# Optimization experiments

Measured on AMD Instinct MI355X. Metric: run time of the kernel, lower is better.

## Reference

```python
import jax, jax.numpy as jnp
import numpy as np

BETA = 0.04
EPS_LOW = 0.2
EPS_HIGH = 0.2
TEMPERATURE = 1.0


def setup_inputs() -> dict:
    key = jax.random.key(0)
    ks = jax.random.split(key, 8)
    B, S, H, V = 4, 1024, 2048, 32000
    return {
        "_input": jax.random.normal(ks[0], (B, S, H), dtype=jnp.float32),
        "lin_weight": jax.random.normal(ks[1], (V, H), dtype=jnp.float32) * 0.02,
        "bias": jax.random.normal(ks[2], (V,), dtype=jnp.float32) * 0.02,
        "selected_token_ids": jax.random.randint(ks[3], (B, S), 0, V),
        "attention_mask": jnp.ones((B, S), dtype=jnp.float32),
        "advantages": jax.random.normal(ks[4], (B,), dtype=jnp.float32),
        "ref_per_token_logps": -jnp.abs(jax.random.normal(ks[5], (B, S), dtype=jnp.float32)),
        "old_per_token_logps": -jnp.abs(jax.random.normal(ks[6], (B, S), dtype=jnp.float32)),
    }


def reference(_input, lin_weight, bias, selected_token_ids, attention_mask,
              advantages, ref_per_token_logps, old_per_token_logps):
    B, S, H = _input.shape
    # fused linear projection to vocab logits: [B,S,V]
    logits = (jnp.einsum("bsh,vh->bsv", _input, lin_weight) + bias) / TEMPERATURE
    log_probs = jax.nn.log_softmax(logits, axis=-1)
    per_token_logps = jnp.take_along_axis(
        log_probs, selected_token_ids[..., None], axis=-1)[..., 0]  # [B,S]

    log_ratio = per_token_logps - old_per_token_logps
    seq_len = jnp.clip(attention_mask.sum(-1), 1.0, None)
    seq_level_log_weight = jax.lax.stop_gradient(
        (log_ratio * attention_mask).sum(-1) / seq_len)[:, None]  # [B,1]

    log_importance_weights = (per_token_logps -
                              jax.lax.stop_gradient(per_token_logps) +
                              seq_level_log_weight)
    coef_1 = jnp.exp(log_importance_weights)
    coef_2 = jnp.clip(coef_1, 1.0 - EPS_LOW, 1.0 + EPS_HIGH)
    adv = advantages[:, None]
    per_token_loss = -jnp.minimum(coef_1 * adv, coef_2 * adv)

    # k3 KL penalty (beta != 0, use_ref_model=True)
    d = ref_per_token_logps - per_token_logps
    kl_div = jnp.exp(d) - d - 1.0
    per_token_loss = per_token_loss + BETA * kl_div

    # loss_type == 'grpo'
    loss = ((per_token_loss * attention_mask).sum(-1) / seq_len).sum() / B
    return loss
```

## Files before the change

kernel.cpp:

```cpp
#include <hip/hip_runtime.h>
#include <hip/hip_bf16.h>

#define BETA_C 0.04f
#define EPS_LOW_C 0.2f
#define EPS_HIGH_C 0.2f

static constexpr int B_ = 4, S_ = 1024, H_ = 2048, V_ = 32000;
static constexpr int M_ = B_ * S_;
static constexpr int BM = 256, BN = 256, BK = 64;
static constexpr int NRB = M_ / BM;
static constexpr int NCB = V_ / BN;
static constexpr int NT  = H_ / BK;

typedef __attribute__((ext_vector_type(8))) short short8;
typedef __attribute__((ext_vector_type(4))) float f32x4;

__device__ __forceinline__ unsigned short f2bf(float f) {
    unsigned u = __builtin_bit_cast(unsigned, f);
    unsigned r = 0x7FFFu + ((u >> 16) & 1u);
    return (unsigned short)((u + r) >> 16);
}

__device__ __forceinline__ void gload_lds16(const unsigned short* g, unsigned short* l) {
    __builtin_amdgcn_global_load_lds(
        (const __attribute__((address_space(1))) unsigned int*)g,
        (__attribute__((address_space(3))) unsigned int*)l, 16, 0, 0);
}

__global__ void cvt_kernel(const float* __restrict__ in, unsigned short* __restrict__ out, int n4) {
    int i = blockIdx.x * blockDim.x + threadIdx.x;
    int stride = gridDim.x * blockDim.x;
    for (; i < n4; i += stride) {
        float4 v = reinterpret_cast<const float4*>(in)[i];
        ushort4 o;
        o.x = f2bf(v.x); o.y = f2bf(v.y); o.z = f2bf(v.z); o.w = f2bf(v.w);
        reinterpret_cast<ushort4*>(out)[i] = o;
    }
}

__global__ __launch_bounds__(512, 2) void gemm_lse_kernel(
    const unsigned short* __restrict__ A,
    const unsigned short* __restrict__ W,
    const float* __restrict__ bias,
    const int* __restrict__ sel,
    float* __restrict__ partials,
    float* __restrict__ sel_logit)
{
    __shared__ __attribute__((aligned(128))) char lds[163840];

    const int bid = blockIdx.x;
    const int swz = (bid & 7) * (NRB * NCB / 8) + (bid >> 3);
    const int brow = swz % NRB;
    const int bcol = swz / NRB;
    const int tid  = threadIdx.x;
    const int lane = tid & 63;
    const int wv   = tid >> 6;
    const int wm   = wv >> 2;
    const int wn   = wv & 3;
    const int l15  = lane & 15, lg = lane >> 4;

    int aBase[2], bBase[2];
    #pragma unroll
    for (int ks = 0; ks < 2; ++ks) {
        const int sw = ((ks * 4 + lg) ^ (l15 & 7)) << 4;
        aBase[ks] = (wm * 128 + l15) * 128 + sw;
        bBase[ks] = (wn * 64 + l15) * 128 + sw;
    }
    int sByte[2][2];
    #pragma unroll
    for (int i = 0; i < 2; ++i)
        #pragma unroll
        for (int h = 0; h < 2; ++h) {
            int c = i * 512 + tid;
            int r = (c >> 3) + h * 128;
            int gg = (c & 7) ^ (r & 7);
            sByte[i][h] = (r * H_ + gg * 8) * 2;
        }

    const unsigned short* Ab = A + (long)brow * BM * H_;
    const unsigned short* Wb = W + (long)bcol * BN * H_;

    f32x4 acc[8][4] = {};
    short8 af0[2][2], af1[2][2], af2[2][2], af3[2][2], bfr[4][2];

#define STG(gb, bufoff, h, kt) \
    { _Pragma("unroll") \
      for (int i_ = 0; i_ < 2; ++i_) \
          gload_lds16((const unsigned short*)((const char*)(gb) + sByte[i_][h] + (kt) * 2), \
                      (unsigned short*)(lds + (bufoff) + (h) * 16384 + (i_ * 512 + tid) * 16)); }

#define RDA(abuf, q, dst) \
    { _Pragma("unroll") \
      for (int mi_ = 0; mi_ < 2; ++mi_) \
      _Pragma("unroll") \
      for (int ks_ = 0; ks_ < 2; ++ks_) \
          dst[mi_][ks_] = *(const short8*)(lds + (abuf) + ((q) * 2 + mi_) * 2048 + aBase[ks_]); }

#define RDB(bbuf) \
    { _Pragma("unroll") \
      for (int n_ = 0; n_ < 4; ++n_) \
      _Pragma("unroll") \
      for (int ks_ = 0; ks_ < 2; ++ks_) \
          bfr[n_][ks_] = *(const short8*)(lds + (bbuf) + n_ * 2048 + bBase[ks_]); }

#define MM(q, afr) \
    __builtin_amdgcn_s_setprio(1); \
    _Pragma("unroll") \
    for (int ks_ = 0; ks_ < 2; ++ks_) \
    _Pragma("unroll") \
    for (int mi_ = 0; mi_ < 2; ++mi_) \
    _Pragma("unroll") \
    for (int n_ = 0; n_ < 4; ++n_) \
        acc[(q) * 2 + mi_][n_] = __builtin_amdgcn_mfma_f32_16x16x32_bf16( \
            afr[mi_][ks_], bfr[n_][ks_], acc[(q) * 2 + mi_][n_], 0, 0, 0); \
    __builtin_amdgcn_s_setprio(0);

#define LGKM(n) asm volatile("s_waitcnt lgkmcnt(" #n ")" ::: "memory"); \
    __builtin_amdgcn_sched_barrier(0);
#define VMC(n)  asm volatile("s_waitcnt vmcnt(" #n ")" ::: "memory");
#define BAR     { __builtin_amdgcn_s_barrier(); __builtin_amdgcn_sched_barrier(0); }
#define SCB     __builtin_amdgcn_sched_barrier(0);

    STG(Ab, 0, 0, 0)       STG(Ab, 0, 1, 0)
    STG(Wb, 65536, 0, 0)   STG(Wb, 65536, 1, 0)
    STG(Wb, 98304, 0, 64)  STG(Wb, 98304, 1, 64)
    VMC(4)
    BAR

    #pragma unroll
    for (int t = 0; t < NT; ++t) {
        const int aR = (t & 1) * 32768;
        const int aW = ((t + 1) & 1) * 32768;
        const int bR = 65536 + (t % 3) * 32768;
        const int bW = 65536 + ((t + 2) % 3) * 32768;
        const int ktA = ((t + 1) * BK) & (H_ - 1);
        const int ktB = ((t + 2) * BK) & (H_ - 1);

        RDB(bR) RDA(aR, 0, af0)
        SCB
        RDA(aR, 1, af1)
        SCB
        STG(Ab, aW, 0, ktA) STG(Ab, aW, 1, ktA)
        STG(Wb, bW, 0, ktB) STG(Wb, bW, 1, ktB)
        LGKM(4)
        MM(0, af0)
        RDA(aR, 2, af2)
        SCB
        LGKM(4)
        MM(1, af1)
        RDA(aR, 3, af3)
        SCB
        LGKM(4)
        MM(2, af2)
        LGKM(0)
        MM(3, af3)
        VMC(4)
        BAR
    }

    VMC(0)
    __syncthreads();

    float* sums = (float*)lds;
    const int colb = bcol * BN + wn * 64 + l15;
    float bv[4];
    #pragma unroll
    for (int n = 0; n < 4; ++n) bv[n] = bias[colb + n * 16];

    #pragma unroll
    for (int m = 0; m < 8; ++m) {
        #pragma unroll
        for (int j = 0; j < 4; ++j) {
            const long grow = (long)brow * BM + wm * 128 + m * 16 + lg * 4 + j;
            const int stok = sel[grow];
            float s = 0.f;
            #pragma unroll
            for (int n = 0; n < 4; ++n) {
                float logit = acc[m][n][j] + bv[n];
                s += __expf(logit);
                if (stok == colb + n * 16) sel_logit[grow] = logit;
            }
            s += __shfl_xor(s, 1); s += __shfl_xor(s, 2);
            s += __shfl_xor(s, 4); s += __shfl_xor(s, 8);
            if (l15 == 0) sums[(wm * 128 + m * 16 + lg * 4 + j) * 4 + wn] = s;
        }
    }
    __syncthreads();
    if (tid < BM) {
        float tot = sums[tid * 4 + 0] + sums[tid * 4 + 1] + sums[tid * 4 + 2] + sums[tid * 4 + 3];
        partials[((long)brow * BM + tid) * NCB + bcol] = tot;
    }
#undef STG
#undef RDA
#undef RDB
#undef MM
#undef LGKM
#undef VMC
#undef BAR
#undef SCB
}

__global__ void reduce_lse_kernel(const float* __restrict__ partials,
                                  const float* __restrict__ sel_logit,
                                  float* __restrict__ lp) {
    const int row = blockIdx.x;
    const int lane = threadIdx.x;
    float s = 0.f;
    for (int i = lane; i < NCB; i += 64) s += partials[(long)row * NCB + i];
    #pragma unroll
    for (int o = 32; o; o >>= 1) s += __shfl_xor(s, o);
    if (lane == 0) lp[row] = sel_logit[row] - __logf(s);
}

__device__ __forceinline__ float block_sum(float v, float* red) {
    const int lane = threadIdx.x & 63, wid = threadIdx.x >> 6;
    #pragma unroll
    for (int o = 32; o; o >>= 1) v += __shfl_xor(v, o);
    if (lane == 0) red[wid] = v;
    __syncthreads();
    if (wid == 0) {
        float x = (lane < 16) ? red[lane] : 0.f;
        #pragma unroll
        for (int o = 8; o; o >>= 1) x += __shfl_xor(x, o);
        if (lane == 0) red[0] = x;
    }
    __syncthreads();
    float r = red[0];
    __syncthreads();
    return r;
}

__global__ __launch_bounds__(1024) void loss_kernel(
    const float* __restrict__ lp, const float* __restrict__ mask,
    const float* __restrict__ adv, const float* __restrict__ ref,
    const float* __restrict__ old, float* __restrict__ out) {
    __shared__ float red[16];
    const int s = threadIdx.x;
    float loss_acc = 0.f;
    for (int b = 0; b < 4; ++b) {
        const int i = b * S_ + s;
        const float mk = mask[i];
        const float lpv = lp[i];
        const float lrsum = block_sum((lpv - old[i]) * mk, red);
        const float msum  = block_sum(mk, red);
        const float seqlen = fmaxf(msum, 1.f);
        const float sw = lrsum / seqlen;
        const float c1 = __expf(sw);
        const float c2 = fminf(fmaxf(c1, 1.f - EPS_LOW_C), 1.f + EPS_HIGH_C);
        const float a = adv[b];
        const float pmin = fminf(c1 * a, c2 * a);
        const float d = ref[i] - lpv;
        const float ptl = -pmin + BETA_C * (__expf(d) - d - 1.f);
        const float lsum = block_sum(ptl * mk, red);
        loss_acc += lsum / seqlen;
    }
    if (s == 0) out[0] = loss_acc * (1.f / (float)B_);
}

extern "C" void kernel_launch(void* const* d_in, const int* in_sizes, int n_in,
                              void* d_out, int out_size, void* d_ws, size_t ws_size,
                              hipStream_t stream) {
    const float* x    = (const float*)d_in[0];
    const float* W    = (const float*)d_in[1];
    const float* bias = (const float*)d_in[2];
    const int*   sel  = (const int*)d_in[3];
    const float* mask = (const float*)d_in[4];
    const float* adv  = (const float*)d_in[5];
    const float* ref  = (const float*)d_in[6];
    const float* old  = (const float*)d_in[7];
    float* out = (float*)d_out;

    char* ws = (char*)d_ws;
    unsigned short* Abf = (unsigned short*)ws;
    unsigned short* Wbf = (unsigned short*)(ws + 16777216);
    float* partials  = (float*)(ws + 16777216 + 131072000);
    float* sel_logit = (float*)(ws + 16777216 + 131072000 + 2048000);
    float* lp        = sel_logit + M_;

    cvt_kernel<<<2048, 256, 0, stream>>>(x, Abf, M_ * H_ / 4);
    cvt_kernel<<<4096, 256, 0, stream>>>(W, Wbf, V_ * H_ / 4);

    gemm_lse_kernel<<<NRB * NCB, 512, 0, stream>>>(Abf, Wbf, bias, sel, partials, sel_logit);

    reduce_lse_kernel<<<M_, 64, 0, stream>>>(partials, sel_logit, lp);
    loss_kernel<<<1, 1024, 0, stream>>>(lp, mask, adv, ref, old, out);
}
```

Measured before the change: 554.7 us.

## Load W fragments directly from global into registers, bypassing LDS

The B (weight) operand is no longer staged through LDS. Each wave now loads its W fragments straight from global memory into double-buffered registers one K-step ahead, which shrinks LDS from 160KB to 64KB and removes the B-side LDS reads. The cost is that the four N-wave-columns reload overlapping W data without sharing it through LDS. The global loads are also strided per row rather than coalesced, and the pipeline now waits with vmcnt(0) every step instead of keeping two stages in flight, so global latency may be exposed.

```diff
diff --git a/kernel.cpp b/kernel.cpp
--- a/kernel.cpp
+++ b/kernel.cpp
@@ -14,6 +14,7 @@
 
 typedef __attribute__((ext_vector_type(8))) short short8;
 typedef __attribute__((ext_vector_type(4))) float f32x4;
+typedef const __attribute__((address_space(1))) short8* g8p;
 
 __device__ __forceinline__ unsigned short f2bf(float f) {
     unsigned u = __builtin_bit_cast(unsigned, f);
@@ -46,7 +47,7 @@
     float* __restrict__ partials,
     float* __restrict__ sel_logit)
 {
-    __shared__ __attribute__((aligned(128))) char lds[163840];
+    __shared__ __attribute__((aligned(128))) char lds[65536];
 
     const int bid = blockIdx.x;
     const int swz = (bid & 7) * (NRB * NCB / 8) + (bid >> 3);
@@ -59,12 +60,11 @@
     const int wn   = wv & 3;
     const int l15  = lane & 15, lg = lane >> 4;
 
-    int aBase[2], bBase[2];
+    int aBase[2];
     #pragma unroll
     for (int ks = 0; ks < 2; ++ks) {
         const int sw = ((ks * 4 + lg) ^ (l15 & 7)) << 4;
         aBase[ks] = (wm * 128 + l15) * 128 + sw;
-        bBase[ks] = (wn * 64 + l15) * 128 + sw;
     }
     int sByte[2][2];
     #pragma unroll
@@ -80,14 +80,27 @@
     const unsigned short* Ab = A + (long)brow * BM * H_;
     const unsigned short* Wb = W + (long)bcol * BN * H_;
 
+    const unsigned short* bP[4];
+    #pragma unroll
+    for (int n = 0; n < 4; ++n)
+        bP[n] = Wb + (long)(wn * 64 + n * 16 + l15) * H_ + lg * 8;
+
     f32x4 acc[8][4] = {};
-    short8 af0[2][2], af1[2][2], af2[2][2], af3[2][2], bfr[4][2];
+    short8 afA[2][2], afB[2][2];
+    short8 bX[4][2], bY[4][2];
 
 #define STG(gb, bufoff, h, kt) \
     { _Pragma("unroll") \
       for (int i_ = 0; i_ < 2; ++i_) \
           gload_lds16((const unsigned short*)((const char*)(gb) + sByte[i_][h] + (kt) * 2), \
                       (unsigned short*)(lds + (bufoff) + (h) * 16384 + (i_ * 512 + tid) * 16)); }
+
+#define LDB(dst, tt) \
+    { _Pragma("unroll") \
+      for (int n_ = 0; n_ < 4; ++n_) \
+      _Pragma("unroll") \
+      for (int ks_ = 0; ks_ < 2; ++ks_) \
+          dst[n_][ks_] = *(g8p)(bP[n_] + (((tt) * BK + ks_ * 32) & (H_ - 1))); }
 
 #define RDA(abuf, q, dst) \
     { _Pragma("unroll") \
@@ -96,14 +109,7 @@
       for (int ks_ = 0; ks_ < 2; ++ks_) \
           dst[mi_][ks_] = *(const short8*)(lds + (abuf) + ((q) * 2 + mi_) * 2048 + aBase[ks_]); }
 
-#define RDB(bbuf) \
-    { _Pragma("unroll") \
-      for (int n_ = 0; n_ < 4; ++n_) \
-      _Pragma("unroll") \
-      for (int ks_ = 0; ks_ < 2; ++ks_) \
-          bfr[n_][ks_] = *(const short8*)(lds + (bbuf) + n_ * 2048 + bBase[ks_]); }
-
-#define MM(q, afr) \
+#define MM(q, afr, bcur) \
     __builtin_amdgcn_s_setprio(1); \
     _Pragma("unroll") \
     for (int ks_ = 0; ks_ < 2; ++ks_) \
@@ -112,7 +118,7 @@
     _Pragma("unroll") \
     for (int n_ = 0; n_ < 4; ++n_) \
         acc[(q) * 2 + mi_][n_] = __builtin_amdgcn_mfma_f32_16x16x32_bf16( \
-            afr[mi_][ks_], bfr[n_][ks_], acc[(q) * 2 + mi_][n_], 0, 0, 0); \
+            afr[mi_][ks_], bcur[n_][ks_], acc[(q) * 2 + mi_][n_], 0, 0, 0); \
     __builtin_amdgcn_s_setprio(0);
 
 #define LGKM(n) asm volatile("s_waitcnt lgkmcnt(" #n ")" ::: "memory"); \
@@ -121,44 +127,46 @@
 #define BAR     { __builtin_amdgcn_s_barrier(); __builtin_amdgcn_sched_barrier(0); }
 #define SCB     __builtin_amdgcn_sched_barrier(0);
 
-    STG(Ab, 0, 0, 0)       STG(Ab, 0, 1, 0)
-    STG(Wb, 65536, 0, 0)   STG(Wb, 65536, 1, 0)
-    STG(Wb, 98304, 0, 64)  STG(Wb, 98304, 1, 64)
-    VMC(4)
+#define STEP(t, cur, nxt) \
+    { \
+        const int aR = ((t) & 1) * 32768; \
+        const int aW = (((t) + 1) & 1) * 32768; \
+        const int ktA = (((t) + 1) * BK) & (H_ - 1); \
+        LDB(nxt, (t) + 1) \
+        SCB \
+        STG(Ab, aW, 0, ktA) STG(Ab, aW, 1, ktA) \
+        SCB \
+        RDA(aR, 0, afA) \
+        SCB \
+        RDA(aR, 1, afB) \
+        SCB \
+        LGKM(4)   \
+        MM(0, afA, cur) \
+        RDA(aR, 2, afA) \
+        SCB \
+        LGKM(4)   \
+        MM(1, afB, cur) \
+        RDA(aR, 3, afB) \
+        SCB \
+        LGKM(4)   \
+        MM(2, afA, cur) \
+        LGKM(0)   \
+        MM(3, afB, cur) \
+        VMC(0)    \
+        BAR \
+    }
+
+    LDB(bX, 0)
+    STG(Ab, 0, 0, 0) STG(Ab, 0, 1, 0)
+    VMC(0)
     BAR
 
     #pragma unroll
-    for (int t = 0; t < NT; ++t) {
-        const int aR = (t & 1) * 32768;
-        const int aW = ((t + 1) & 1) * 32768;
-        const int bR = 65536 + (t % 3) * 32768;
-        const int bW = 65536 + ((t + 2) % 3) * 32768;
-        const int ktA = ((t + 1) * BK) & (H_ - 1);
-        const int ktB = ((t + 2) * BK) & (H_ - 1);
-
-        RDB(bR) RDA(aR, 0, af0)
-        SCB
-        RDA(aR, 1, af1)
-        SCB
-        STG(Ab, aW, 0, ktA) STG(Ab, aW, 1, ktA)
-        STG(Wb, bW, 0, ktB) STG(Wb, bW, 1, ktB)
-        LGKM(4)
-        MM(0, af0)
-        RDA(aR, 2, af2)
-        SCB
-        LGKM(4)
-        MM(1, af1)
-        RDA(aR, 3, af3)
-        SCB
-        LGKM(4)
-        MM(2, af2)
-        LGKM(0)
-        MM(3, af3)
-        VMC(4)
-        BAR
-    }
-
-    VMC(0)
+    for (int t = 0; t < NT; t += 2) {
+        STEP(t, bX, bY)
+        STEP(t + 1, bY, bX)
+    }
+
     __syncthreads();
 
     float* sums = (float*)lds;
@@ -191,13 +199,14 @@
         partials[((long)brow * BM + tid) * NCB + bcol] = tot;
     }
 #undef STG
+#undef LDB
 #undef RDA
-#undef RDB
 #undef MM
 #undef LGKM
 #undef VMC
 #undef BAR
 #undef SCB
+#undef STEP
 }
 
 __global__ void reduce_lse_kernel(const float* __restrict__ partials,
```

Result: slower. 837.7 us (+51.0%).
